# Performance work log

Measured on AMD Instinct MI355X. Metric: run time of the kernel, lower is better.

## Reference

```python
import jax, jax.numpy as jnp
import numpy as np

B, C, H, W = 32, 192, 56, 56
DILATIONS = (1, 3, 5)
EPS = 1e-5


def setup_inputs() -> dict:
    key = jax.random.key(0)
    ks = jax.random.split(key, 4)
    x = jax.random.normal(ks[0], (B, C, H, W), dtype=jnp.float32)
    # learned params (per original torch init where it matters for math)
    bias = jnp.zeros((1, C, 1, 1), dtype=jnp.float32)            # LearnableBias
    conv_w = jax.random.normal(ks[1], (3, C, 1, 3, 3), dtype=jnp.float32) * 0.1  # depthwise kernels (OIHW, I=1)
    conv_b = jax.random.normal(ks[2], (3, C), dtype=jnp.float32) * 0.01
    move1 = jnp.zeros((3, C), dtype=jnp.float32)
    alpha = jnp.full((3, C), 0.25, dtype=jnp.float32)            # PReLU default init
    move2 = jnp.zeros((3, C), dtype=jnp.float32)
    ln_gamma = jnp.ones((C,), dtype=jnp.float32)
    ln_beta = jnp.zeros((C,), dtype=jnp.float32)
    return {"x": x, "bias": bias, "conv_w": conv_w, "conv_b": conv_b,
            "move1": move1, "alpha": alpha, "move2": move2,
            "ln_gamma": ln_gamma, "ln_beta": ln_beta}


def _per_ch(v):
    # (C,) -> (1,C,1,1) broadcastable over NCHW
    return v[None, :, None, None]


def reference(x, bias, conv_w, conv_b, move1, alpha, move2, ln_gamma, ln_beta):
    c = x.shape[1]
    xb = x + bias  # LearnableBias
    out = jnp.zeros_like(x)
    for i, d in enumerate(DILATIONS):
        # depthwise 3x3 dilated conv, 'same' padding => pad = d for k=3
        y = jax.lax.conv_general_dilated(
            xb, conv_w[i],
            window_strides=(1, 1),
            padding=((d, d), (d, d)),
            rhs_dilation=(d, d),
            feature_group_count=c,
            dimension_numbers=("NCHW", "OIHW", "NCHW"),
        ) + _per_ch(conv_b[i])
        # RPReLU: shift, per-channel PReLU, shift
        y = y - _per_ch(move1[i])
        y = jnp.where(y >= 0, y, _per_ch(alpha[i]) * y)
        y = y + _per_ch(move2[i])
        out = out + y
    # LayerNorm over channel dim (torch applies it on NHWC last axis == channels)
    mean = out.mean(axis=1, keepdims=True)
    var = out.var(axis=1, keepdims=True)  # biased, matches torch LayerNorm
    out = (out - mean) * jax.lax.rsqrt(var + EPS)
    out = out * _per_ch(ln_gamma) + _per_ch(ln_beta)
    return out
```

## Files before the change

### kernel.cpp

```cpp
#include <hip/hip_runtime.h>

#define C 192
#define H 56
#define W 56
#define HW (H * W)
#define CHW (C * HW)
#define NB 32
#define PPS 36
#define EPSLN 1e-5f

#define CTL_SHL1 0x101
#define CTL_SHL2 0x102
#define CTL_SHR1 0x111
#define CTL_SHR2 0x112

template<int CTRL>
__device__ __forceinline__ float dppf(float v) {
    return __int_as_float(__builtin_amdgcn_update_dpp(
        0, __float_as_int(v), CTRL, 0xf, 0xf, true));
}

struct __attribute__((aligned(16))) f4 { float x, y, z, w; };

__device__ __forceinline__ f4 f4z() { return {0.f, 0.f, 0.f, 0.f}; }
__device__ __forceinline__ f4 f4b(float s) { return {s, s, s, s}; }
__device__ __forceinline__ f4 fma4(f4 a, float s, f4 c) {
    return { fmaf(a.x, s, c.x), fmaf(a.y, s, c.y),
             fmaf(a.z, s, c.z), fmaf(a.w, s, c.w) };
}
__device__ __forceinline__ f4 shp1(f4 v){ return { v.y, v.z, v.w, dppf<CTL_SHL1>(v.x) }; }
__device__ __forceinline__ f4 shm1(f4 v){ return { dppf<CTL_SHR1>(v.w), v.x, v.y, v.z }; }
__device__ __forceinline__ f4 shp3(f4 v){ return { v.w, dppf<CTL_SHL1>(v.x),
                                                   dppf<CTL_SHL1>(v.y), dppf<CTL_SHL1>(v.z) }; }
__device__ __forceinline__ f4 shm3(f4 v){ return { dppf<CTL_SHR1>(v.y), dppf<CTL_SHR1>(v.z),
                                                   dppf<CTL_SHR1>(v.w), v.x }; }
__device__ __forceinline__ f4 shp5(f4 v){ return { dppf<CTL_SHL1>(v.y), dppf<CTL_SHL1>(v.z),
                                                   dppf<CTL_SHL1>(v.w), dppf<CTL_SHL2>(v.x) }; }
__device__ __forceinline__ f4 shm5(f4 v){ return { dppf<CTL_SHR2>(v.w), dppf<CTL_SHR1>(v.x),
                                                   dppf<CTL_SHR1>(v.y), dppf<CTL_SHR1>(v.z) }; }

__device__ __forceinline__ f4 prelu_acc(f4 acc, f4 y, float a) {
    acc.x += fmaxf(y.x, 0.f) + a * fminf(y.x, 0.f);
    acc.y += fmaxf(y.y, 0.f) + a * fminf(y.y, 0.f);
    acc.z += fmaxf(y.z, 0.f) + a * fminf(y.z, 0.f);
    acc.w += fmaxf(y.w, 0.f) + a * fminf(y.w, 0.f);
    return acc;
}

__global__ void prep_kernel(const float* __restrict__ bias,
                            const float* __restrict__ conv_w,
                            const float* __restrict__ conv_b,
                            const float* __restrict__ move1,
                            const float* __restrict__ alpha,
                            const float* __restrict__ move2,
                            const float* __restrict__ ln_g,
                            const float* __restrict__ ln_b,
                            float* __restrict__ pp, float* __restrict__ gb) {
    const int c = threadIdx.x;
    if (c >= C) return;
    float* pc = pp + c * PPS;
    #pragma unroll
    for (int i = 0; i < 3; ++i)
        #pragma unroll
        for (int k = 0; k < 9; ++k)
            pc[i * 9 + k] = conv_w[(size_t)(i * C + c) * 9 + k];
    #pragma unroll
    for (int i = 0; i < 3; ++i) {
        pc[27 + i] = conv_b[i * C + c] - move1[i * C + c];
        pc[30 + i] = alpha[i * C + c];
    }
    pc[33] = bias[c];
    pc[34] = move2[0 * C + c] + move2[1 * C + c] + move2[2 * C + c];
    pc[35] = 0.f;
    gb[2 * c]     = ln_g[c];
    gb[2 * c + 1] = ln_b[c];
}

__global__ __launch_bounds__(256, 3) void msgdc_kernel(
    const float* __restrict__ x, const float* __restrict__ pp,
    const float* __restrict__ gb, float* __restrict__ out)
{
    __shared__ float tile[C * W];
    __shared__ float sred[4][16][8];

    const int t = threadIdx.x;
    const int lane = t & 63;
    const int wv = __builtin_amdgcn_readfirstlane(t >> 6);
    const int l = lane & 15;
    const bool act = (l < 14);
    const float act_f = act ? 1.f : 0.f;
    const int lw = act ? 4 * l : 52;

    const int blk = blockIdx.x;
    const int gid = (blk & 7) * 224 + (blk >> 3);
    const int b = gid / H;
    const int h = gid - b * H;

    const bool vr[7] = { h >= 5, h >= 3, h >= 1, true,
                         h <= H - 2, h <= H - 4, h <= H - 6 };
    const int  ro[7] = { -5 * W, -3 * W, -1 * W, 0, 1 * W, 3 * W, 5 * W };
    float vm[7];
    #pragma unroll
    for (int k = 0; k < 7; ++k) vm[k] = vr[k] ? 1.f : 0.f;

    const int cbase = wv * 48 + (lane >> 4);
    const float* xc = x + (size_t)b * CHW + (size_t)cbase * HW + h * W + lw;

    f4 cur[7], nxt[7];
    #pragma unroll
    for (int k = 0; k < 7; ++k)
        nxt[k] = vr[k] ? *(const f4*)(xc + ro[k]) : f4z();

    f4 s4 = f4z(), q4 = f4z();

    #pragma unroll 2
    for (int j = 0; j < 12; ++j) {
        const int c = cbase + 4 * j;
        #pragma unroll
        for (int k = 0; k < 7; ++k) cur[k] = nxt[k];

        const float* pc = pp + c * PPS;
        float wf[36];
        #pragma unroll
        for (int k = 0; k < 9; ++k)
            *(f4*)(wf + 4 * k) = *(const f4*)(pc + 4 * k);

        if (j < 11) {
            const float* xn = xc + (size_t)(4 * (j + 1)) * HW;
            #pragma unroll
            for (int k = 0; k < 7; ++k)
                nxt[k] = vr[k] ? *(const f4*)(xn + ro[k]) : f4z();
        }

        const float bs = wf[33];
        f4 r[7];
        #pragma unroll
        for (int k = 0; k < 7; ++k) {
            const float bk = bs * vm[k] * act_f;
            r[k].x = fmaf(cur[k].x, act_f, bk);
            r[k].y = fmaf(cur[k].y, act_f, bk);
            r[k].z = fmaf(cur[k].z, act_f, bk);
            r[k].w = fmaf(cur[k].w, act_f, bk);
        }

        f4 acc = f4b(wf[34]);
        {
            f4 y = f4b(wf[27]);
            y = fma4(shm1(r[2]), wf[0], y);
            y = fma4(r[2],       wf[1], y);
            y = fma4(shp1(r[2]), wf[2], y);
            y = fma4(shm1(r[3]), wf[3], y);
            y = fma4(r[3],       wf[4], y);
            y = fma4(shp1(r[3]), wf[5], y);
            y = fma4(shm1(r[4]), wf[6], y);
            y = fma4(r[4],       wf[7], y);
            y = fma4(shp1(r[4]), wf[8], y);
            acc = prelu_acc(acc, y, wf[30]);
        }
        {
            f4 y = f4b(wf[28]);
            y = fma4(shm3(r[1]), wf[9],  y);
            y = fma4(r[1],       wf[10], y);
            y = fma4(shp3(r[1]), wf[11], y);
            y = fma4(shm3(r[3]), wf[12], y);
            y = fma4(r[3],       wf[13], y);
            y = fma4(shp3(r[3]), wf[14], y);
            y = fma4(shm3(r[5]), wf[15], y);
            y = fma4(r[5],       wf[16], y);
            y = fma4(shp3(r[5]), wf[17], y);
            acc = prelu_acc(acc, y, wf[31]);
        }
        {
            f4 y = f4b(wf[29]);
            y = fma4(shm5(r[0]), wf[18], y);
            y = fma4(r[0],       wf[19], y);
            y = fma4(shp5(r[0]), wf[20], y);
            y = fma4(shm5(r[3]), wf[21], y);
            y = fma4(r[3],       wf[22], y);
            y = fma4(shp5(r[3]), wf[23], y);
            y = fma4(shm5(r[6]), wf[24], y);
            y = fma4(r[6],       wf[25], y);
            y = fma4(shp5(r[6]), wf[26], y);
            acc = prelu_acc(acc, y, wf[32]);
        }

        s4.x += acc.x; s4.y += acc.y; s4.z += acc.z; s4.w += acc.w;
        q4.x = fmaf(acc.x, acc.x, q4.x); q4.y = fmaf(acc.y, acc.y, q4.y);
        q4.z = fmaf(acc.z, acc.z, q4.z); q4.w = fmaf(acc.w, acc.w, q4.w);

        if (act) *(f4*)(tile + c * W + lw) = acc;
    }

    #pragma unroll
    for (int m = 16; m <= 32; m <<= 1) {
        s4.x += __shfl_xor(s4.x, m, 64); s4.y += __shfl_xor(s4.y, m, 64);
        s4.z += __shfl_xor(s4.z, m, 64); s4.w += __shfl_xor(s4.w, m, 64);
        q4.x += __shfl_xor(q4.x, m, 64); q4.y += __shfl_xor(q4.y, m, 64);
        q4.z += __shfl_xor(q4.z, m, 64); q4.w += __shfl_xor(q4.w, m, 64);
    }
    if (lane < 14) {
        *(f4*)&sred[wv][lane][0] = s4;
        *(f4*)&sred[wv][lane][4] = q4;
    }
    __syncthreads();

    f4 S = f4z(), Q = f4z();
    #pragma unroll
    for (int w2 = 0; w2 < 4; ++w2) {
        const f4 a = *(const f4*)&sred[w2][l][0];
        const f4 bq = *(const f4*)&sred[w2][l][4];
        S.x += a.x; S.y += a.y; S.z += a.z; S.w += a.w;
        Q.x += bq.x; Q.y += bq.y; Q.z += bq.z; Q.w += bq.w;
    }
    const float inv = 1.f / (float)C;
    f4 mean = { S.x * inv, S.y * inv, S.z * inv, S.w * inv };
    f4 rstd = { rsqrtf(Q.x * inv - mean.x * mean.x + EPSLN),
                rsqrtf(Q.y * inv - mean.y * mean.y + EPSLN),
                rsqrtf(Q.z * inv - mean.z * mean.z + EPSLN),
                rsqrtf(Q.w * inv - mean.w * mean.w + EPSLN) };

    float* ob = out + (size_t)b * CHW + (size_t)cbase * HW + h * W + lw;
    #pragma unroll 2
    for (int j = 0; j < 12; ++j) {
        const int c = cbase + 4 * j;
        const float ga = gb[2 * c], be = gb[2 * c + 1];
        if (act) {
            const f4 v = *(const f4*)(tile + c * W + lw);
            f4 o;
            o.x = fmaf((v.x - mean.x) * rstd.x, ga, be);
            o.y = fmaf((v.y - mean.y) * rstd.y, ga, be);
            o.z = fmaf((v.z - mean.z) * rstd.z, ga, be);
            o.w = fmaf((v.w - mean.w) * rstd.w, ga, be);
            *(f4*)(ob + (size_t)(4 * j) * HW) = o;
        }
    }
}

extern "C" void kernel_launch(void* const* d_in, const int* in_sizes, int n_in,
                              void* d_out, int out_size, void* d_ws, size_t ws_size,
                              hipStream_t stream) {
    const float* x       = (const float*)d_in[0];
    const float* bias    = (const float*)d_in[1];
    const float* conv_w  = (const float*)d_in[2];
    const float* conv_b  = (const float*)d_in[3];
    const float* move1   = (const float*)d_in[4];
    const float* alpha   = (const float*)d_in[5];
    const float* move2   = (const float*)d_in[6];
    const float* ln_g    = (const float*)d_in[7];
    const float* ln_b    = (const float*)d_in[8];
    float* out = (float*)d_out;

    float* pp = (float*)d_ws;
    float* gbp = pp + C * PPS;

    prep_kernel<<<1, 256, 0, stream>>>(bias, conv_w, conv_b, move1, alpha,
                                       move2, ln_g, ln_b, pp, gbp);
    msgdc_kernel<<<NB * H, 256, 0, stream>>>(x, pp, gbp, out);
}
```

Before: 204.3 us.

## Keep last four channel results in registers, shrink LDS tile, raise occupancy

The first 8 of each thread's 12 channels are staged in a smaller shared tile. The last 4 channel results stay in registers until the LayerNorm statistics are ready. This shrinks LDS per block from 192 to 128 channel rows, and launch bounds go from 3 to 5 blocks per CU so more blocks can be resident. Output stores become nontemporal to avoid polluting the cache. The cost is more register pressure from holding four extra vectors under a tighter register budget, which risks spills.

```diff
diff --git a/kernel.cpp b/kernel.cpp
--- a/kernel.cpp
+++ b/kernel.cpp
@@ -21,6 +21,7 @@
 }
 
 struct __attribute__((aligned(16))) f4 { float x, y, z, w; };
+typedef __attribute__((ext_vector_type(4))) float v4f;
 
 __device__ __forceinline__ f4 f4z() { return {0.f, 0.f, 0.f, 0.f}; }
 __device__ __forceinline__ f4 f4b(float s) { return {s, s, s, s}; }
@@ -76,17 +77,18 @@
     gb[2 * c + 1] = ln_b[c];
 }
 
-__global__ __launch_bounds__(256, 3) void msgdc_kernel(
+__global__ __launch_bounds__(256, 5) void msgdc_kernel(
     const float* __restrict__ x, const float* __restrict__ pp,
     const float* __restrict__ gb, float* __restrict__ out)
 {
-    __shared__ float tile[C * W];
+    __shared__ float tile[128 * W];
     __shared__ float sred[4][16][8];
 
     const int t = threadIdx.x;
     const int lane = t & 63;
     const int wv = __builtin_amdgcn_readfirstlane(t >> 6);
     const int l = lane & 15;
+    const int tix = wv * 4 + (lane >> 4);
     const bool act = (l < 14);
     const float act_f = act ? 1.f : 0.f;
     const int lw = act ? 4 * l : 52;
@@ -113,19 +115,15 @@
 
     f4 s4 = f4z(), q4 = f4z();
 
-    #pragma unroll 2
-    for (int j = 0; j < 12; ++j) {
+    auto step = [&](int j, bool pf) -> f4 {
         const int c = cbase + 4 * j;
-        #pragma unroll
-        for (int k = 0; k < 7; ++k) cur[k] = nxt[k];
-
         const float* pc = pp + c * PPS;
         float wf[36];
         #pragma unroll
         for (int k = 0; k < 9; ++k)
             *(f4*)(wf + 4 * k) = *(const f4*)(pc + 4 * k);
 
-        if (j < 11) {
+        if (pf) {
             const float* xn = xc + (size_t)(4 * (j + 1)) * HW;
             #pragma unroll
             for (int k = 0; k < 7; ++k)
@@ -187,8 +185,22 @@
         s4.x += acc.x; s4.y += acc.y; s4.z += acc.z; s4.w += acc.w;
         q4.x = fmaf(acc.x, acc.x, q4.x); q4.y = fmaf(acc.y, acc.y, q4.y);
         q4.z = fmaf(acc.z, acc.z, q4.z); q4.w = fmaf(acc.w, acc.w, q4.w);
-
-        if (act) *(f4*)(tile + c * W + lw) = acc;
+        return acc;
+    };
+
+    #pragma unroll 2
+    for (int j = 0; j < 8; ++j) {
+        #pragma unroll
+        for (int k = 0; k < 7; ++k) cur[k] = nxt[k];
+        f4 acc = step(j, true);
+        if (act) *(f4*)(tile + (tix * 8 + j) * W + lw) = acc;
+    }
+    f4 acc_r[4];
+    #pragma unroll
+    for (int jj = 0; jj < 4; ++jj) {
+        #pragma unroll
+        for (int k = 0; k < 7; ++k) cur[k] = nxt[k];
+        acc_r[jj] = step(8 + jj, jj < 3);
     }
 
     #pragma unroll
@@ -221,17 +233,31 @@
 
     float* ob = out + (size_t)b * CHW + (size_t)cbase * HW + h * W + lw;
     #pragma unroll 2
-    for (int j = 0; j < 12; ++j) {
+    for (int j = 0; j < 8; ++j) {
         const int c = cbase + 4 * j;
         const float ga = gb[2 * c], be = gb[2 * c + 1];
         if (act) {
-            const f4 v = *(const f4*)(tile + c * W + lw);
-            f4 o;
+            const f4 v = *(const f4*)(tile + (tix * 8 + j) * W + lw);
+            v4f o;
             o.x = fmaf((v.x - mean.x) * rstd.x, ga, be);
             o.y = fmaf((v.y - mean.y) * rstd.y, ga, be);
             o.z = fmaf((v.z - mean.z) * rstd.z, ga, be);
             o.w = fmaf((v.w - mean.w) * rstd.w, ga, be);
-            *(f4*)(ob + (size_t)(4 * j) * HW) = o;
+            __builtin_nontemporal_store(o, (v4f*)(ob + (size_t)(4 * j) * HW));
+        }
+    }
+    #pragma unroll
+    for (int jj = 0; jj < 4; ++jj) {
+        const int c = cbase + 32 + 4 * jj;
+        const float ga = gb[2 * c], be = gb[2 * c + 1];
+        if (act) {
+            const f4 v = acc_r[jj];
+            v4f o;
+            o.x = fmaf((v.x - mean.x) * rstd.x, ga, be);
+            o.y = fmaf((v.y - mean.y) * rstd.y, ga, be);
+            o.z = fmaf((v.z - mean.z) * rstd.z, ga, be);
+            o.w = fmaf((v.w - mean.w) * rstd.w, ga, be);
+            __builtin_nontemporal_store(o, (v4f*)(ob + (size_t)(32 + 4 * jj) * HW));
         }
     }
 }
```

Result: slower. 543.1 us (+165.8%).

## Keep last four channel results in registers to shrink LDS tile and raise occupancy

Applied to the files above, without the earlier changes.

The kernel keeps the last 4 of each thread's 12 channel results in registers and stores only the first 8 in shared memory. The shared tile shrinks from 192 to 128 channel rows, and launch bounds go from 3 to 4 blocks per SIMD set. Output stores now use nontemporal hints. The aim is more resident blocks to hide memory latency, at the cost of register pressure that could cause spills under the tighter launch bound.

```diff
diff --git a/kernel.cpp b/kernel.cpp
--- a/kernel.cpp
+++ b/kernel.cpp
@@ -21,6 +21,7 @@
 }
 
 struct __attribute__((aligned(16))) f4 { float x, y, z, w; };
+typedef __attribute__((ext_vector_type(4))) float v4f;
 
 __device__ __forceinline__ f4 f4z() { return {0.f, 0.f, 0.f, 0.f}; }
 __device__ __forceinline__ f4 f4b(float s) { return {s, s, s, s}; }
@@ -76,17 +77,92 @@
     gb[2 * c + 1] = ln_b[c];
 }
 
-__global__ __launch_bounds__(256, 3) void msgdc_kernel(
+#define STEP_BODY(JV, DO_PF, ACC_OUT)                                        \
+    {                                                                        \
+        const int c_ = cbase + 4 * (JV);                                     \
+        const float* pc_ = pp + c_ * PPS;                                    \
+        float wf[36];                                                        \
+        _Pragma("unroll")                                                    \
+        for (int k = 0; k < 9; ++k)                                          \
+            *(f4*)(wf + 4 * k) = *(const f4*)(pc_ + 4 * k);                  \
+        if (DO_PF) {                                                         \
+            const float* xn_ = xc + (size_t)(4 * ((JV) + 1)) * HW;           \
+            _Pragma("unroll")                                                \
+            for (int k = 0; k < 7; ++k)                                      \
+                nxt[k] = vr[k] ? *(const f4*)(xn_ + ro[k]) : f4z();          \
+        }                                                                    \
+        const float bs_ = wf[33];                                            \
+        f4 r[7];                                                             \
+        _Pragma("unroll")                                                    \
+        for (int k = 0; k < 7; ++k) {                                        \
+            const float bk_ = bs_ * vm[k] * act_f;                           \
+            r[k].x = fmaf(cur[k].x, act_f, bk_);                             \
+            r[k].y = fmaf(cur[k].y, act_f, bk_);                             \
+            r[k].z = fmaf(cur[k].z, act_f, bk_);                             \
+            r[k].w = fmaf(cur[k].w, act_f, bk_);                             \
+        }                                                                    \
+        f4 acc_ = f4b(wf[34]);                                               \
+        {                                                         \
+            f4 y = f4b(wf[27]);                                              \
+            y = fma4(shm1(r[2]), wf[0], y);                                  \
+            y = fma4(r[2],       wf[1], y);                                  \
+            y = fma4(shp1(r[2]), wf[2], y);                                  \
+            y = fma4(shm1(r[3]), wf[3], y);                                  \
+            y = fma4(r[3],       wf[4], y);                                  \
+            y = fma4(shp1(r[3]), wf[5], y);                                  \
+            y = fma4(shm1(r[4]), wf[6], y);                                  \
+            y = fma4(r[4],       wf[7], y);                                  \
+            y = fma4(shp1(r[4]), wf[8], y);                                  \
+            acc_ = prelu_acc(acc_, y, wf[30]);                               \
+        }                                                                    \
+        {                                                         \
+            f4 y = f4b(wf[28]);                                              \
+            y = fma4(shm3(r[1]), wf[9],  y);                                 \
+            y = fma4(r[1],       wf[10], y);                                 \
+            y = fma4(shp3(r[1]), wf[11], y);                                 \
+            y = fma4(shm3(r[3]), wf[12], y);                                 \
+            y = fma4(r[3],       wf[13], y);                                 \
+            y = fma4(shp3(r[3]), wf[14], y);                                 \
+            y = fma4(shm3(r[5]), wf[15], y);                                 \
+            y = fma4(r[5],       wf[16], y);                                 \
+            y = fma4(shp3(r[5]), wf[17], y);                                 \
+            acc_ = prelu_acc(acc_, y, wf[31]);                               \
+        }                                                                    \
+        {                                                         \
+            f4 y = f4b(wf[29]);                                              \
+            y = fma4(shm5(r[0]), wf[18], y);                                 \
+            y = fma4(r[0],       wf[19], y);                                 \
+            y = fma4(shp5(r[0]), wf[20], y);                                 \
+            y = fma4(shm5(r[3]), wf[21], y);                                 \
+            y = fma4(r[3],       wf[22], y);                                 \
+            y = fma4(shp5(r[3]), wf[23], y);                                 \
+            y = fma4(shm5(r[6]), wf[24], y);                                 \
+            y = fma4(r[6],       wf[25], y);                                 \
+            y = fma4(shp5(r[6]), wf[26], y);                                 \
+            acc_ = prelu_acc(acc_, y, wf[32]);                               \
+        }                                                                    \
+        s4.x += acc_.x; s4.y += acc_.y; s4.z += acc_.z; s4.w += acc_.w;      \
+        q4.x = fmaf(acc_.x, acc_.x, q4.x); q4.y = fmaf(acc_.y, acc_.y, q4.y);\
+        q4.z = fmaf(acc_.z, acc_.z, q4.z); q4.w = fmaf(acc_.w, acc_.w, q4.w);\
+        (ACC_OUT) = acc_;                                                    \
+    }
+
+#define ROTATE_CUR()                                                         \
+    _Pragma("unroll")                                                        \
+    for (int k = 0; k < 7; ++k) cur[k] = nxt[k];
+
+__global__ __launch_bounds__(256, 4) void msgdc_kernel(
     const float* __restrict__ x, const float* __restrict__ pp,
     const float* __restrict__ gb, float* __restrict__ out)
 {
-    __shared__ float tile[C * W];
+    __shared__ float tile[128 * W];
     __shared__ float sred[4][16][8];
 
     const int t = threadIdx.x;
     const int lane = t & 63;
     const int wv = __builtin_amdgcn_readfirstlane(t >> 6);
     const int l = lane & 15;
+    const int tix = wv * 4 + (lane >> 4);
     const bool act = (l < 14);
     const float act_f = act ? 1.f : 0.f;
     const int lw = act ? 4 * l : 52;
@@ -114,82 +190,17 @@
     f4 s4 = f4z(), q4 = f4z();
 
     #pragma unroll 2
-    for (int j = 0; j < 12; ++j) {
-        const int c = cbase + 4 * j;
-        #pragma unroll
-        for (int k = 0; k < 7; ++k) cur[k] = nxt[k];
-
-        const float* pc = pp + c * PPS;
-        float wf[36];
-        #pragma unroll
-        for (int k = 0; k < 9; ++k)
-            *(f4*)(wf + 4 * k) = *(const f4*)(pc + 4 * k);
-
-        if (j < 11) {
-            const float* xn = xc + (size_t)(4 * (j + 1)) * HW;
-            #pragma unroll
-            for (int k = 0; k < 7; ++k)
-                nxt[k] = vr[k] ? *(const f4*)(xn + ro[k]) : f4z();
-        }
-
-        const float bs = wf[33];
-        f4 r[7];
-        #pragma unroll
-        for (int k = 0; k < 7; ++k) {
-            const float bk = bs * vm[k] * act_f;
-            r[k].x = fmaf(cur[k].x, act_f, bk);
-            r[k].y = fmaf(cur[k].y, act_f, bk);
-            r[k].z = fmaf(cur[k].z, act_f, bk);
-            r[k].w = fmaf(cur[k].w, act_f, bk);
-        }
-
-        f4 acc = f4b(wf[34]);
-        {
-            f4 y = f4b(wf[27]);
-            y = fma4(shm1(r[2]), wf[0], y);
-            y = fma4(r[2],       wf[1], y);
-            y = fma4(shp1(r[2]), wf[2], y);
-            y = fma4(shm1(r[3]), wf[3], y);
-            y = fma4(r[3],       wf[4], y);
-            y = fma4(shp1(r[3]), wf[5], y);
-            y = fma4(shm1(r[4]), wf[6], y);
-            y = fma4(r[4],       wf[7], y);
-            y = fma4(shp1(r[4]), wf[8], y);
-            acc = prelu_acc(acc, y, wf[30]);
-        }
-        {
-            f4 y = f4b(wf[28]);
-            y = fma4(shm3(r[1]), wf[9],  y);
-            y = fma4(r[1],       wf[10], y);
-            y = fma4(shp3(r[1]), wf[11], y);
-            y = fma4(shm3(r[3]), wf[12], y);
-            y = fma4(r[3],       wf[13], y);
-            y = fma4(shp3(r[3]), wf[14], y);
-            y = fma4(shm3(r[5]), wf[15], y);
-            y = fma4(r[5],       wf[16], y);
-            y = fma4(shp3(r[5]), wf[17], y);
-            acc = prelu_acc(acc, y, wf[31]);
-        }
-        {
-            f4 y = f4b(wf[29]);
-            y = fma4(shm5(r[0]), wf[18], y);
-            y = fma4(r[0],       wf[19], y);
-            y = fma4(shp5(r[0]), wf[20], y);
-            y = fma4(shm5(r[3]), wf[21], y);
-            y = fma4(r[3],       wf[22], y);
-            y = fma4(shp5(r[3]), wf[23], y);
-            y = fma4(shm5(r[6]), wf[24], y);
-            y = fma4(r[6],       wf[25], y);
-            y = fma4(shp5(r[6]), wf[26], y);
-            acc = prelu_acc(acc, y, wf[32]);
-        }
-
-        s4.x += acc.x; s4.y += acc.y; s4.z += acc.z; s4.w += acc.w;
-        q4.x = fmaf(acc.x, acc.x, q4.x); q4.y = fmaf(acc.y, acc.y, q4.y);
-        q4.z = fmaf(acc.z, acc.z, q4.z); q4.w = fmaf(acc.w, acc.w, q4.w);
-
-        if (act) *(f4*)(tile + c * W + lw) = acc;
-    }
+    for (int j = 0; j < 8; ++j) {
+        ROTATE_CUR();
+        f4 acc;
+        STEP_BODY(j, true, acc);
+        if (act) *(f4*)(tile + (tix * 8 + j) * W + lw) = acc;
+    }
+    f4 acc_r0, acc_r1, acc_r2, acc_r3;
+    { ROTATE_CUR(); STEP_BODY(8,  true,  acc_r0); }
+    { ROTATE_CUR(); STEP_BODY(9,  true,  acc_r1); }
+    { ROTATE_CUR(); STEP_BODY(10, true,  acc_r2); }
+    { ROTATE_CUR(); STEP_BODY(11, false, acc_r3); }
 
     #pragma unroll
     for (int m = 16; m <= 32; m <<= 1) {
@@ -221,19 +232,39 @@
 
     float* ob = out + (size_t)b * CHW + (size_t)cbase * HW + h * W + lw;
     #pragma unroll 2
-    for (int j = 0; j < 12; ++j) {
+    for (int j = 0; j < 8; ++j) {
         const int c = cbase + 4 * j;
         const float ga = gb[2 * c], be = gb[2 * c + 1];
         if (act) {
-            const f4 v = *(const f4*)(tile + c * W + lw);
-            f4 o;
+            const f4 v = *(const f4*)(tile + (tix * 8 + j) * W + lw);
+            v4f o;
             o.x = fmaf((v.x - mean.x) * rstd.x, ga, be);
             o.y = fmaf((v.y - mean.y) * rstd.y, ga, be);
             o.z = fmaf((v.z - mean.z) * rstd.z, ga, be);
             o.w = fmaf((v.w - mean.w) * rstd.w, ga, be);
-            *(f4*)(ob + (size_t)(4 * j) * HW) = o;
+            __builtin_nontemporal_store(o, (v4f*)(ob + (size_t)(4 * j) * HW));
         }
     }
+#define LN_REG_STORE(JJ, ACCV)                                               \
+    {                                                                        \
+        const int c_ = cbase + 4 * (8 + (JJ));                               \
+        const float ga_ = gb[2 * c_], be_ = gb[2 * c_ + 1];                  \
+        if (act) {                                                           \
+            const f4 v = (ACCV);                                             \
+            v4f o;                                                           \
+            o.x = fmaf((v.x - mean.x) * rstd.x, ga_, be_);                   \
+            o.y = fmaf((v.y - mean.y) * rstd.y, ga_, be_);                   \
+            o.z = fmaf((v.z - mean.z) * rstd.z, ga_, be_);                   \
+            o.w = fmaf((v.w - mean.w) * rstd.w, ga_, be_);                   \
+            __builtin_nontemporal_store(o,                                   \
+                (v4f*)(ob + (size_t)(4 * (8 + (JJ))) * HW));                 \
+        }                                                                    \
+    }
+    LN_REG_STORE(0, acc_r0);
+    LN_REG_STORE(1, acc_r1);
+    LN_REG_STORE(2, acc_r2);
+    LN_REG_STORE(3, acc_r3);
+#undef LN_REG_STORE
 }
 
 extern "C" void kernel_launch(void* const* d_in, const int* in_sizes, int n_in,
```

Measured after the change: 402.1 us. +96.8%, slower.
